# Optimization experiments

Hardware: AMD Instinct MI355X
Metric: run time of the kernel (lower is better)

## Reference

```python
import jax, jax.numpy as jnp
import numpy as np

NUM_CLASSES = 19
K = 100                 # max_views_per_class
TEMP = 0.1
BASE_TEMP = 0.07
EPS_NORM = 1e-12


def _l2_normalize(x):
    # matches torch F.normalize(dim=1): x / max(||x||, eps)
    n = jnp.sqrt(jnp.sum(x * x, axis=1, keepdims=True))
    return x / jnp.maximum(n, EPS_NORM)


def _sample_indices(labels_flat):
    # Deterministic per-class sampler: first K pixels of each class.
    # (torch version uses randperm; the downstream math is identical.)
    # Every class is guaranteed >= K pixels by input construction.
    idxs = [jnp.where(labels_flat == c, size=K, fill_value=0)[0]
            for c in range(NUM_CLASSES)]
    return jnp.concatenate(idxs)  # [NUM_CLASSES*K]


def setup_inputs() -> dict:
    key = jax.random.key(0)
    k1, k2, k3, k4 = jax.random.split(key, 4)
    pixel_feats = jax.random.normal(k1, (8, 256, 128, 128), dtype=jnp.float32)
    labels = jax.random.randint(k2, (8, 128, 128), 0, NUM_CLASSES).astype(jnp.int64)
    memory_feats = jax.random.normal(k3, (20000, 256), dtype=jnp.float32)
    memory_labels = jax.random.randint(k4, (20000,), 0, NUM_CLASSES).astype(jnp.int64)
    return {"pixel_feats": pixel_feats, "labels": labels,
            "memory_feats": memory_feats, "memory_labels": memory_labels}


def reference(pixel_feats, labels, memory_feats, memory_labels):
    B, D, H, W = pixel_feats.shape
    feats_flat = pixel_feats.transpose(0, 2, 3, 1).reshape(-1, D)   # [B*H*W, D]
    labels_flat = labels.reshape(-1)

    idx = _sample_indices(labels_flat)
    anchor_feats = feats_flat[idx]                                  # [Na, D]
    anchor_labels = jnp.repeat(jnp.arange(NUM_CLASSES), K)          # [Na]

    contrast_feats = jnp.concatenate([anchor_feats, memory_feats], axis=0)
    contrast_labels = jnp.concatenate([anchor_labels, memory_labels], axis=0)

    a = _l2_normalize(anchor_feats)
    c = _l2_normalize(contrast_feats)
    logits = jnp.einsum('nd,md->nm', a, c) / TEMP                   # [Na, Nc]

    Na, Nc = logits.shape
    mask = (anchor_labels[:, None] == contrast_labels[None, :]).astype(logits.dtype)
    # remove self-contrast (diagonal of the first Na contrast columns)
    rows = jnp.arange(Na)
    logits_mask = jnp.ones((Na, Nc), dtype=logits.dtype).at[rows, rows].set(0.0)
    mask = mask * logits_mask

    exp_logits = jnp.exp(logits) * logits_mask
    log_prob = logits - jnp.log(exp_logits.sum(axis=1, keepdims=True) + 1e-12)

    pos_count = mask.sum(axis=1)                                    # [Na]
    valid = pos_count > 0
    mean_log_prob_pos = (mask * log_prob).sum(axis=1) / jnp.maximum(pos_count, 1.0)
    n_valid = jnp.maximum(jnp.sum(valid).astype(logits.dtype), 1.0)
    loss = -(TEMP / BASE_TEMP) * (jnp.sum(jnp.where(valid, mean_log_prob_pos, 0.0)) / n_valid)
    return loss
```

## Files before the change

kernel.cpp:

```cpp
#include <hip/hip_runtime.h>
#include <hip/hip_bf16.h>
#include <math.h>

#define NCLS   19
#define KPC    100
#define NA     1900
#define NM     20000
#define NC     21900
#define NCP2   22016
#define D      256
#define HW     16384
#define NPIX   131072
#define NT_M   15
#define NT_N   172
#define NTILES (NT_M * NT_N)

#define B_SAMPLE 0
#define B_MEM    19
#define B_CLAB   2519
#define B_PAD    2605
#define B_ZERO   2620
#define K1_GRID  2621

typedef __attribute__((ext_vector_type(8))) short bf16x8;
typedef __attribute__((ext_vector_type(4))) float f32x4;

#define WS_ROWS  64
#define WS_ROWP  7744
#define WS_IDX   15424
#define WS_CLAB  30720
#define WS_CT2   118784

__device__ __forceinline__ short f2bf(float x) {
    __hip_bfloat16 h = __float2bfloat16(x);
    return *(short*)&h;
}

__global__ void prep_kernel(const int* __restrict__ labels, const float* __restrict__ mem,
                            const int* __restrict__ memlab,
                            int* __restrict__ idx, int* __restrict__ clab,
                            short* __restrict__ Ct2,
                            float* __restrict__ rowS, float* __restrict__ rowP) {
    const int b = blockIdx.x;
    const int t = threadIdx.x;
    if (b < B_MEM) {
        const int c = b;
        const int wave = t >> 6, lane = t & 63;
        __shared__ int s_base;
        __shared__ int s_wavecnt[4];
        if (t == 0) s_base = 0;
        __syncthreads();
        for (int start = 0; start < NPIX; start += 256) {
            const int i = start + t;
            const bool pred = (labels[i] == c);
            const unsigned long long bm = __ballot(pred);
            if (lane == 0) s_wavecnt[wave] = __popcll(bm);
            __syncthreads();
            const int base = s_base;
            int wbase = 0;
            for (int w = 0; w < wave; ++w) wbase += s_wavecnt[w];
            const int chunk_total = s_wavecnt[0] + s_wavecnt[1] + s_wavecnt[2] + s_wavecnt[3];
            if (pred) {
                const int rank = base + wbase + __popcll(bm & ((1ULL << lane) - 1ULL));
                if (rank < KPC) idx[c * KPC + rank] = i;
            }
            __syncthreads();
            if (t == 0) s_base = base + chunk_total;
            if (base + chunk_total >= KPC) break;
        }
    } else if (b < B_CLAB) {
        const int r  = (b - B_MEM) * 8 + (t >> 5);
        const int kq = t & 31;
        const float4 v0 = *(const float4*)(mem + (size_t)r * D + kq * 8);
        const float4 v1 = *(const float4*)(mem + (size_t)r * D + kq * 8 + 4);
        float ssq = v0.x*v0.x + v0.y*v0.y + v0.z*v0.z + v0.w*v0.w
                  + v1.x*v1.x + v1.y*v1.y + v1.z*v1.z + v1.w*v1.w;
        #pragma unroll
        for (int o = 16; o; o >>= 1) ssq += __shfl_xor(ssq, o, 32);
        const float inv = 1.0f / fmaxf(sqrtf(ssq), 1e-12f);
        bf16x8 ov;
        ov[0] = f2bf(v0.x * inv); ov[1] = f2bf(v0.y * inv);
        ov[2] = f2bf(v0.z * inv); ov[3] = f2bf(v0.w * inv);
        ov[4] = f2bf(v1.x * inv); ov[5] = f2bf(v1.y * inv);
        ov[6] = f2bf(v1.z * inv); ov[7] = f2bf(v1.w * inv);
        *(bf16x8*)(Ct2 + ((size_t)kq * NCP2 + NA + r) * 8) = ov;
    } else if (b < B_PAD) {
        const int i = (b - B_CLAB) * 256 + t;
        clab[i] = (i < NA) ? ((i * 5243) >> 19)
                           : ((i < NC) ? memlab[i - NA] : -1);
    } else if (b < B_ZERO) {
        const int e = (b - B_PAD) * 256 + t;
        if (e < 32 * (NCP2 - NC)) {
            const int kq = e / (NCP2 - NC);
            const int n  = NC + (e - kq * (NCP2 - NC));
            bf16x8 z = {};
            *(bf16x8*)(Ct2 + ((size_t)kq * NCP2 + n) * 8) = z;
        }
    } else {
        for (int i = t; i < 1920; i += 256) { rowS[i] = 0.f; rowP[i] = 0.f; }
    }
}

__global__ void anchor_kernel(const float* __restrict__ pixel, const int* __restrict__ idx,
                              short* __restrict__ Ct2) {
    const int t = threadIdx.x;
    const int a = blockIdx.x * 8 + (t >> 5);
    const int kq = t & 31;
    if (a >= NA) return;
    const int p = idx[a];
    const int bi = p >> 14;
    const int hw = p & (HW - 1);
    const float* base = pixel + ((size_t)(bi * D + kq * 8)) * HW + hw;
    float v[8];
    float ssq = 0.f;
    #pragma unroll
    for (int j = 0; j < 8; ++j) { v[j] = base[(size_t)j * HW]; ssq += v[j] * v[j]; }
    #pragma unroll
    for (int o = 16; o; o >>= 1) ssq += __shfl_xor(ssq, o, 32);
    const float inv = 1.0f / fmaxf(sqrtf(ssq), 1e-12f);
    bf16x8 ov;
    #pragma unroll
    for (int j = 0; j < 8; ++j) ov[j] = f2bf(v[j] * inv);
    *(bf16x8*)(Ct2 + ((size_t)kq * NCP2 + a) * 8) = ov;
}

__global__ __launch_bounds__(256, 3)
void mfma_gemm_kernel(const short* __restrict__ Ct2, const int* __restrict__ clab,
                      float* __restrict__ rowS, float* __restrict__ rowP) {
    __shared__ __align__(16) short As[8 * 128 * 8];
    __shared__ __align__(16) short Bs[8 * 128 * 8];
    __shared__ int s_nlab[128];
    const int tid  = threadIdx.x;
    const int lane = tid & 63;
    const int w    = tid >> 6;
    const int wm   = w >> 1, wn = w & 1;
    const int quad = lane >> 4;
    const int l16  = lane & 15;

    const int bid = blockIdx.x;
    const int x   = bid & 7;
    const int j   = bid >> 3;
    const int wg  = (x < 4 ? x * 323 : 1292 + (x - 4) * 322) + j;
    const int m0  = (wg % NT_M) * 128;
    const int n0  = (wg / NT_M) * 128;

    f32x4 acc[4][4] = {};

    for (int kc = 0; kc < 4; ++kc) {
        #pragma unroll
        for (int i = 0; i < 4; ++i) {
            const int bl = (w * 4 + i) * 64;
            const int kq = bl >> 7;
            const int ml = bl & 127;
            const size_t gA = ((size_t)(kc * 8 + kq) * NCP2 + m0 + ml + lane) * 8;
            __builtin_amdgcn_global_load_lds(
                (const __attribute__((address_space(1))) void*)(Ct2 + gA),
                (__attribute__((address_space(3))) void*)(As + (size_t)bl * 8 + lane * 8),
                16, 0, 0);
            const size_t gB = ((size_t)(kc * 8 + kq) * NCP2 + n0 + ml + lane) * 8;
            __builtin_amdgcn_global_load_lds(
                (const __attribute__((address_space(1))) void*)(Ct2 + gB),
                (__attribute__((address_space(3))) void*)(Bs + (size_t)bl * 8 + lane * 8),
                16, 0, 0);
        }
        __syncthreads();
        #pragma unroll
        for (int ks = 0; ks < 2; ++ks) {
            const int kqb = ks * 4 + quad;
            bf16x8 af[4], bfr[4];
            #pragma unroll
            for (int mi = 0; mi < 4; ++mi)
                af[mi] = *(const bf16x8*)(As + ((kqb * 128) + wm * 64 + mi * 16 + l16) * 8);
            #pragma unroll
            for (int ni = 0; ni < 4; ++ni)
                bfr[ni] = *(const bf16x8*)(Bs + ((kqb * 128) + wn * 64 + ni * 16 + l16) * 8);
            #pragma unroll
            for (int ni = 0; ni < 4; ++ni)
                #pragma unroll
                for (int mi = 0; mi < 4; ++mi)
                    acc[ni][mi] = __builtin_amdgcn_mfma_f32_16x16x32_bf16(
                        bfr[ni], af[mi], acc[ni][mi], 0, 0, 0);
        }
        __syncthreads();
    }

    if (tid < 128) s_nlab[tid] = clab[n0 + tid];
    __syncthreads();

    const int m_base = m0 + wm * 64 + l16;
    #pragma unroll
    for (int mi = 0; mi < 4; ++mi) {
        const int m    = m_base + mi * 16;
        const int mlab = (m * 5243) >> 19;
        float s = 0.f, p = 0.f;
        #pragma unroll
        for (int ni = 0; ni < 4; ++ni) {
            const int nb = wn * 64 + ni * 16 + quad * 4;
            const int4 lb = *(const int4*)&s_nlab[nb];
            #pragma unroll
            for (int r = 0; r < 4; ++r) {
                const int n  = n0 + nb + r;
                const int nl = (&lb.x)[r];
                if (n < NC && n != m) {
                    const float l = acc[ni][mi][r] * 10.0f;
                    s += __expf(l);
                    if (nl == mlab) p += l;
                }
            }
        }
        s += __shfl_xor(s, 16, 64); s += __shfl_xor(s, 32, 64);
        p += __shfl_xor(p, 16, 64); p += __shfl_xor(p, 32, 64);
        if (quad == 0 && m < NA) {
            atomicAdd(&rowS[m], s);
            atomicAdd(&rowP[m], p);
        }
    }
}

__global__ void finalize_kernel(const float* __restrict__ rowS, const float* __restrict__ rowP,
                                const int* __restrict__ memlab, float* __restrict__ out) {
    const int t = threadIdx.x;
    __shared__ int hist[NCLS];
    __shared__ float rs[4], rn[4];
    if (t < NCLS) hist[t] = 0;
    __syncthreads();
    for (int i = t; i < NM; i += 256) atomicAdd(&hist[memlab[i]], 1);
    __syncthreads();
    float sum = 0.f, nval = 0.f;
    for (int n = t; n < NA; n += 256) {
        const float cnt  = (float)(KPC - 1 + hist[(n * 5243) >> 19]);
        const float logS = logf(rowS[n] + 1e-12f);
        const float mean = (rowP[n] - cnt * logS) / fmaxf(cnt, 1.0f);
        if (cnt > 0.f) { sum += mean; nval += 1.f; }
    }
    for (int o = 32; o; o >>= 1) {
        sum  += __shfl_xor(sum, o, 64);
        nval += __shfl_xor(nval, o, 64);
    }
    if ((t & 63) == 0) { rs[t >> 6] = sum; rn[t >> 6] = nval; }
    __syncthreads();
    if (t == 0) {
        const float s  = rs[0] + rs[1] + rs[2] + rs[3];
        const float nv = rn[0] + rn[1] + rn[2] + rn[3];
        out[0] = -(0.1f / 0.07f) * (s / fmaxf(nv, 1.f));
    }
}

extern "C" void kernel_launch(void* const* d_in, const int* in_sizes, int n_in,
                              void* d_out, int out_size, void* d_ws, size_t ws_size,
                              hipStream_t stream) {
    const float* pixel  = (const float*)d_in[0];
    const int*   labels = (const int*)d_in[1];
    const float* mem    = (const float*)d_in[2];
    const int*   memlab = (const int*)d_in[3];
    char* ws = (char*)d_ws;
    float* rowS = (float*)(ws + WS_ROWS);
    float* rowP = (float*)(ws + WS_ROWP);
    int*   idx  = (int*)(ws + WS_IDX);
    int*   clab = (int*)(ws + WS_CLAB);
    short* Ct2  = (short*)(ws + WS_CT2);
    float* out  = (float*)d_out;

    prep_kernel<<<dim3(K1_GRID), dim3(256), 0, stream>>>(
        labels, mem, memlab, idx, clab, Ct2, rowS, rowP);
    anchor_kernel<<<dim3(238), dim3(256), 0, stream>>>(pixel, idx, Ct2);
    mfma_gemm_kernel<<<dim3(NTILES), dim3(256), 0, stream>>>(Ct2, clab, rowS, rowP);
    finalize_kernel<<<dim3(1), dim3(256), 0, stream>>>(rowS, rowP, memlab, out);
}
```

Before: 242.2 us.

## Load GEMM fragments directly from global memory, dropping LDS staging

The MFMA GEMM kernel no longer stages A and B tiles through shared memory with global_load_lds and barriers. Each wave now loads its bf16x8 fragments straight from global memory (relying on L2/L1 for reuse across waves) in a fully unrolled K loop. Launch bounds rise to 4 blocks per SM. This removes LDS traffic and the per-chunk synchronisation. In exchange each fragment is fetched from global memory by two waves, and register pressure goes up.

```diff
diff --git a/kernel.cpp b/kernel.cpp
--- a/kernel.cpp
+++ b/kernel.cpp
@@ -124,11 +124,9 @@
     *(bf16x8*)(Ct2 + ((size_t)kq * NCP2 + a) * 8) = ov;
 }
 
-__global__ __launch_bounds__(256, 3)
+__global__ __launch_bounds__(256, 4)
 void mfma_gemm_kernel(const short* __restrict__ Ct2, const int* __restrict__ clab,
                       float* __restrict__ rowS, float* __restrict__ rowP) {
-    __shared__ __align__(16) short As[8 * 128 * 8];
-    __shared__ __align__(16) short Bs[8 * 128 * 8];
     __shared__ int s_nlab[128];
     const int tid  = threadIdx.x;
     const int lane = tid & 63;
@@ -144,47 +142,32 @@
     const int m0  = (wg % NT_M) * 128;
     const int n0  = (wg / NT_M) * 128;
 
+    if (tid < 128) s_nlab[tid] = clab[n0 + tid];
+
+    const int aCol = m0 + wm * 64 + l16;
+    const int bCol = n0 + wn * 64 + l16;
+
     f32x4 acc[4][4] = {};
 
-    for (int kc = 0; kc < 4; ++kc) {
-        #pragma unroll
-        for (int i = 0; i < 4; ++i) {
-            const int bl = (w * 4 + i) * 64;
-            const int kq = bl >> 7;
-            const int ml = bl & 127;
-            const size_t gA = ((size_t)(kc * 8 + kq) * NCP2 + m0 + ml + lane) * 8;
-            __builtin_amdgcn_global_load_lds(
-                (const __attribute__((address_space(1))) void*)(Ct2 + gA),
-                (__attribute__((address_space(3))) void*)(As + (size_t)bl * 8 + lane * 8),
-                16, 0, 0);
-            const size_t gB = ((size_t)(kc * 8 + kq) * NCP2 + n0 + ml + lane) * 8;
-            __builtin_amdgcn_global_load_lds(
-                (const __attribute__((address_space(1))) void*)(Ct2 + gB),
-                (__attribute__((address_space(3))) void*)(Bs + (size_t)bl * 8 + lane * 8),
-                16, 0, 0);
-        }
-        __syncthreads();
-        #pragma unroll
-        for (int ks = 0; ks < 2; ++ks) {
-            const int kqb = ks * 4 + quad;
-            bf16x8 af[4], bfr[4];
+    #pragma unroll
+    for (int kb = 0; kb < 8; ++kb) {
+        const int kqb = kb * 4 + quad;
+        const short* kbase = Ct2 + (size_t)kqb * NCP2 * 8;
+        bf16x8 af[4], bfr[4];
+        #pragma unroll
+        for (int mi = 0; mi < 4; ++mi)
+            af[mi] = *(const bf16x8*)(kbase + (size_t)(aCol + mi * 16) * 8);
+        #pragma unroll
+        for (int ni = 0; ni < 4; ++ni)
+            bfr[ni] = *(const bf16x8*)(kbase + (size_t)(bCol + ni * 16) * 8);
+        #pragma unroll
+        for (int ni = 0; ni < 4; ++ni)
             #pragma unroll
             for (int mi = 0; mi < 4; ++mi)
-                af[mi] = *(const bf16x8*)(As + ((kqb * 128) + wm * 64 + mi * 16 + l16) * 8);
-            #pragma unroll
-            for (int ni = 0; ni < 4; ++ni)
-                bfr[ni] = *(const bf16x8*)(Bs + ((kqb * 128) + wn * 64 + ni * 16 + l16) * 8);
-            #pragma unroll
-            for (int ni = 0; ni < 4; ++ni)
-                #pragma unroll
-                for (int mi = 0; mi < 4; ++mi)
-                    acc[ni][mi] = __builtin_amdgcn_mfma_f32_16x16x32_bf16(
-                        bfr[ni], af[mi], acc[ni][mi], 0, 0, 0);
-        }
-        __syncthreads();
-    }
-
-    if (tid < 128) s_nlab[tid] = clab[n0 + tid];
+                acc[ni][mi] = __builtin_amdgcn_mfma_f32_16x16x32_bf16(
+                    bfr[ni], af[mi], acc[ni][mi], 0, 0, 0);
+    }
+
     __syncthreads();
 
     const int m_base = m0 + wm * 64 + l16;
```

New measurement: 242.7 us. Within noise of the previous version (+0.2%).
